# Kernel tuning notes

Measured on AMD Instinct MI355X. Metric: run time of the kernel, lower is better.

Reference implementation:

```python
import jax, jax.numpy as jnp
import numpy as np

TEMP = 1.0

def setup_inputs() -> dict:
    key = jax.random.key(0)
    k1, k2, k3, k4 = jax.random.split(key, 4)
    B, Q, K, H = 8, 1024, 4096, 512
    output = jax.random.normal(k1, (B, Q, H), dtype=jnp.float32)
    context = jax.random.normal(k2, (B, K, H), dtype=jnp.float32)
    mask = jax.random.randint(k3, (B, Q, K), 0, 2).astype(jnp.bool_)
    # linear_out: Linear(2H -> H), torch layout W: [H, 2H]
    W_out = jax.random.normal(k4, (H, 2 * H), dtype=jnp.float32) * (1.0 / np.sqrt(2 * H))
    b_out = jnp.zeros((H,), dtype=jnp.float32)
    return {"output": output, "context": context, "mask": mask, "W_out": W_out, "b_out": b_out}

def reference(output, context, mask, W_out, b_out):
    # attn scores: [B, Q, K]
    attn = jnp.einsum('bqh,bkh->bqk', output, context)
    attn = jnp.where(mask, -jnp.inf, attn)
    attn = jax.nn.softmax(attn / TEMP, axis=-1)
    # mix: [B, Q, H]
    mix = jnp.einsum('bqk,bkh->bqh', attn, context)
    combined = jnp.concatenate([mix, output], axis=-1)  # [B, Q, 2H]
    out = jnp.tanh(jnp.einsum('bqc,hc->bqh', combined, W_out) + b_out)
    return (out, attn)
```

## Files before the change

### kernel.cpp

```cpp
#include <hip/hip_runtime.h>
#include <cstdint>
#include <cstddef>

#define B_N 8
#define Q_N 1024
#define K_N 4096
#define H_N 512
#define C_N 1024
#define R_N (B_N * Q_N)

typedef short bf16x8 __attribute__((ext_vector_type(8)));
typedef float f32x4 __attribute__((ext_vector_type(4)));

typedef const void __attribute__((address_space(1))) gas_void;
typedef void __attribute__((address_space(3))) las_void;

__device__ __forceinline__ unsigned short f2bf(float f) {
    union { float f; unsigned u; } v; v.f = f;
    unsigned u = v.u;
    u += 0x7FFFu + ((u >> 16) & 1u);
    return (unsigned short)(u >> 16);
}
__device__ __forceinline__ float bf2f(unsigned short h) {
    union { unsigned u; float f; } v; v.u = ((unsigned)h) << 16;
    return v.f;
}

__device__ __forceinline__ f32x4 mfma16(bf16x8 a, bf16x8 b, f32x4 c) {
    return __builtin_amdgcn_mfma_f32_16x16x32_bf16(a, b, c, 0, 0, 0);
}

__global__ void k_split(const float* __restrict__ x, unsigned short* __restrict__ hi,
                        unsigned short* __restrict__ lo, int n4) {
    int i = blockIdx.x * 256 + threadIdx.x;
    if (i >= n4) return;
    float4 v = reinterpret_cast<const float4*>(x)[i];
    ushort4 h, l;
    h.x = f2bf(v.x); l.x = f2bf(v.x - bf2f(h.x));
    h.y = f2bf(v.y); l.y = f2bf(v.y - bf2f(h.y));
    h.z = f2bf(v.z); l.z = f2bf(v.z - bf2f(h.z));
    h.w = f2bf(v.w); l.w = f2bf(v.w - bf2f(h.w));
    reinterpret_cast<ushort4*>(hi)[i] = h;
    reinterpret_cast<ushort4*>(lo)[i] = l;
}

__global__ void k_cvt(const float* __restrict__ x, unsigned short* __restrict__ hi, int n4) {
    int i = blockIdx.x * 256 + threadIdx.x;
    if (i >= n4) return;
    float4 v = reinterpret_cast<const float4*>(x)[i];
    ushort4 h;
    h.x = f2bf(v.x); h.y = f2bf(v.y); h.z = f2bf(v.z); h.w = f2bf(v.w);
    reinterpret_cast<ushort4*>(hi)[i] = h;
}

__global__ void k_transpose(const unsigned short* __restrict__ src, unsigned short* __restrict__ dst) {
    __shared__ unsigned short tile[32][33];
    const int b = blockIdx.z;
    const int k0 = blockIdx.x * 32;
    const int h0 = blockIdx.y * 32;
    const unsigned short* s = src + (size_t)b * K_N * H_N;
    unsigned short* d = dst + (size_t)b * H_N * K_N;
    const int tx = threadIdx.x & 31;
    const int ty = threadIdx.x >> 5;
#pragma unroll
    for (int r = 0; r < 32; r += 8)
        tile[ty + r][tx] = s[(size_t)(k0 + ty + r) * H_N + (h0 + tx)];
    __syncthreads();
#pragma unroll
    for (int r = 0; r < 32; r += 8)
        d[(size_t)(h0 + ty + r) * K_N + (k0 + tx)] = tile[tx][ty + r];
}

__device__ __forceinline__ void stage_tile(const unsigned short* __restrict__ g, int ld,
                                           unsigned short* __restrict__ lds) {
    const int t = threadIdx.x;
    const int wbase = t & ~63;
#pragma unroll
    for (int i = 0; i < 2; i++) {
        int idx = i * 256 + t;
        const unsigned short* ga = g + (size_t)(idx >> 2) * ld + (idx & 3) * 8;
        unsigned short* la = lds + (size_t)(i * 256 + wbase) * 8;
        __builtin_amdgcn_global_load_lds((gas_void*)ga, (las_void*)la, 16, 0, 0);
    }
}

__global__ __launch_bounds__(256, 2)
void k_scores(const unsigned short* __restrict__ outHi, const unsigned short* __restrict__ outLo,
              const unsigned short* __restrict__ ctxHi, const unsigned short* __restrict__ ctxLo,
              float* __restrict__ S) {
    __shared__ unsigned short Ah[128 * 32], Al[128 * 32], Bh[128 * 32], Bl[128 * 32];
    const int b = blockIdx.z;
    const int q0 = blockIdx.y * 128;
    const int k0 = blockIdx.x * 128;
    const unsigned short* Ahg = outHi + ((size_t)b * Q_N + q0) * H_N;
    const unsigned short* Alg = outLo + ((size_t)b * Q_N + q0) * H_N;
    const unsigned short* Bhg = ctxHi + ((size_t)b * K_N + k0) * H_N;
    const unsigned short* Blg = ctxLo + ((size_t)b * K_N + k0) * H_N;
    const int lane = threadIdx.x & 63;
    const int w = threadIdx.x >> 6;
    const int wr = (w >> 1) * 64;
    const int wc = (w & 1) * 64;
    const int fm = lane & 15;
    const int fg = (lane >> 4) * 8;

    f32x4 acc[4][4];
#pragma unroll
    for (int i = 0; i < 4; i++)
#pragma unroll
        for (int j = 0; j < 4; j++) acc[i][j] = (f32x4){0.f, 0.f, 0.f, 0.f};

    for (int kc = 0; kc < H_N; kc += 32) {
        stage_tile(Ahg + kc, H_N, Ah);
        stage_tile(Alg + kc, H_N, Al);
        stage_tile(Bhg + kc, H_N, Bh);
        stage_tile(Blg + kc, H_N, Bl);
        __syncthreads();
        bf16x8 ah[4], al[4], bh[4], bl[4];
#pragma unroll
        for (int i = 0; i < 4; i++) {
            ah[i] = *(const bf16x8*)&Ah[(wr + i * 16 + fm) * 32 + fg];
            al[i] = *(const bf16x8*)&Al[(wr + i * 16 + fm) * 32 + fg];
            bh[i] = *(const bf16x8*)&Bh[(wc + i * 16 + fm) * 32 + fg];
            bl[i] = *(const bf16x8*)&Bl[(wc + i * 16 + fm) * 32 + fg];
        }
#pragma unroll
        for (int i = 0; i < 4; i++)
#pragma unroll
            for (int j = 0; j < 4; j++) {
                acc[i][j] = mfma16(ah[i], bh[j], acc[i][j]);
                acc[i][j] = mfma16(ah[i], bl[j], acc[i][j]);
                acc[i][j] = mfma16(al[i], bh[j], acc[i][j]);
            }
        __syncthreads();
    }
    float* Sb = S + (size_t)b * Q_N * K_N;
    const int orow = (lane >> 4) * 4;
    const int ocol = lane & 15;
#pragma unroll
    for (int i = 0; i < 4; i++)
#pragma unroll
        for (int r = 0; r < 4; r++) {
            int q = q0 + wr + i * 16 + orow + r;
            float* dst = Sb + (size_t)q * K_N + (k0 + wc + ocol);
#pragma unroll
            for (int j = 0; j < 4; j++) dst[j * 16] = acc[i][j][r];
        }
}

__global__ __launch_bounds__(256)
void k_softmax(float* __restrict__ S, const int* __restrict__ mask, unsigned short* __restrict__ pbf) {
    const size_t r = blockIdx.x;
    float* row = S + r * K_N;
    const int* mrow = mask + r * K_N;
    unsigned short* prow = pbf + r * K_N;
    const int t = threadIdx.x;

    float4 v[4];
    float lmax = -1e30f;
#pragma unroll
    for (int i = 0; i < 4; i++) {
        int idx = i * 256 + t;
        float4 s = reinterpret_cast<const float4*>(row)[idx];
        int4 mk = reinterpret_cast<const int4*>(mrow)[idx];
        s.x = mk.x ? -1e30f : s.x;
        s.y = mk.y ? -1e30f : s.y;
        s.z = mk.z ? -1e30f : s.z;
        s.w = mk.w ? -1e30f : s.w;
        v[i] = s;
        lmax = fmaxf(fmaxf(fmaxf(lmax, s.x), fmaxf(s.y, s.z)), s.w);
    }
#pragma unroll
    for (int off = 32; off >= 1; off >>= 1)
        lmax = fmaxf(lmax, __shfl_xor(lmax, off, 64));
    __shared__ float redm[4];
    __shared__ float reds[4];
    const int wv = t >> 6;
    if ((t & 63) == 0) redm[wv] = lmax;
    __syncthreads();
    const float m = fmaxf(fmaxf(redm[0], redm[1]), fmaxf(redm[2], redm[3]));

    float4 e[4];
    float lsum = 0.f;
#pragma unroll
    for (int i = 0; i < 4; i++) {
        e[i].x = __expf(v[i].x - m);
        e[i].y = __expf(v[i].y - m);
        e[i].z = __expf(v[i].z - m);
        e[i].w = __expf(v[i].w - m);
        lsum += (e[i].x + e[i].y) + (e[i].z + e[i].w);
    }
#pragma unroll
    for (int off = 32; off >= 1; off >>= 1)
        lsum += __shfl_xor(lsum, off, 64);
    if ((t & 63) == 0) reds[wv] = lsum;
    __syncthreads();
    const float inv = 1.0f / (reds[0] + reds[1] + reds[2] + reds[3]);

#pragma unroll
    for (int i = 0; i < 4; i++) {
        int idx = i * 256 + t;
        float4 p;
        p.x = e[i].x * inv; p.y = e[i].y * inv; p.z = e[i].z * inv; p.w = e[i].w * inv;
        reinterpret_cast<float4*>(row)[idx] = p;
        ushort4 pb;
        pb.x = f2bf(p.x); pb.y = f2bf(p.y); pb.z = f2bf(p.z); pb.w = f2bf(p.w);
        reinterpret_cast<ushort4*>(prow)[idx] = pb;
    }
}

__global__ __launch_bounds__(256, 2)
void k_mix(const unsigned short* __restrict__ P, const unsigned short* __restrict__ ctxT,
           unsigned short* __restrict__ mixBf) {
    __shared__ unsigned short At[128 * 32], Bt[128 * 32];
    const int b = blockIdx.z;
    const int q0 = blockIdx.y * 128;
    const int h0 = blockIdx.x * 128;
    const unsigned short* Ag = P + ((size_t)b * Q_N + q0) * K_N;
    const unsigned short* Bg = ctxT + ((size_t)b * H_N + h0) * K_N;
    const int lane = threadIdx.x & 63;
    const int w = threadIdx.x >> 6;
    const int wr = (w >> 1) * 64;
    const int wc = (w & 1) * 64;
    const int fm = lane & 15;
    const int fg = (lane >> 4) * 8;

    f32x4 acc[4][4];
#pragma unroll
    for (int i = 0; i < 4; i++)
#pragma unroll
        for (int j = 0; j < 4; j++) acc[i][j] = (f32x4){0.f, 0.f, 0.f, 0.f};

    for (int kc = 0; kc < K_N; kc += 32) {
        stage_tile(Ag + kc, K_N, At);
        stage_tile(Bg + kc, K_N, Bt);
        __syncthreads();
        bf16x8 a[4], bb[4];
#pragma unroll
        for (int i = 0; i < 4; i++) {
            a[i] = *(const bf16x8*)&At[(wr + i * 16 + fm) * 32 + fg];
            bb[i] = *(const bf16x8*)&Bt[(wc + i * 16 + fm) * 32 + fg];
        }
#pragma unroll
        for (int i = 0; i < 4; i++)
#pragma unroll
            for (int j = 0; j < 4; j++) acc[i][j] = mfma16(a[i], bb[j], acc[i][j]);
        __syncthreads();
    }
    const int orow = (lane >> 4) * 4;
    const int ocol = lane & 15;
#pragma unroll
    for (int i = 0; i < 4; i++)
#pragma unroll
        for (int r = 0; r < 4; r++) {
            int q = q0 + wr + i * 16 + orow + r;
            unsigned short* dst = mixBf + ((size_t)b * Q_N + q) * H_N + (h0 + wc + ocol);
#pragma unroll
            for (int j = 0; j < 4; j++) dst[j * 16] = f2bf(acc[i][j][r]);
        }
}

__global__ __launch_bounds__(256, 2)
void k_outlin(const unsigned short* __restrict__ mixBf, const unsigned short* __restrict__ outHi,
              const unsigned short* __restrict__ Whi, const float* __restrict__ bias,
              float* __restrict__ out) {
    __shared__ unsigned short At[128 * 32], Bt[128 * 32];
    const int r0 = blockIdx.y * 128;
    const int h0 = blockIdx.x * 128;
    const int lane = threadIdx.x & 63;
    const int w = threadIdx.x >> 6;
    const int wr = (w >> 1) * 64;
    const int wc = (w & 1) * 64;
    const int fm = lane & 15;
    const int fg = (lane >> 4) * 8;

    f32x4 acc[4][4];
#pragma unroll
    for (int i = 0; i < 4; i++)
#pragma unroll
        for (int j = 0; j < 4; j++) acc[i][j] = (f32x4){0.f, 0.f, 0.f, 0.f};

    for (int kc = 0; kc < C_N; kc += 32) {
        const unsigned short* Ag = (kc < H_N)
            ? mixBf + (size_t)r0 * H_N + kc
            : outHi + (size_t)r0 * H_N + (kc - H_N);
        stage_tile(Ag, H_N, At);
        stage_tile(Whi + (size_t)h0 * C_N + kc, C_N, Bt);
        __syncthreads();
        bf16x8 a[4], bb[4];
#pragma unroll
        for (int i = 0; i < 4; i++) {
            a[i] = *(const bf16x8*)&At[(wr + i * 16 + fm) * 32 + fg];
            bb[i] = *(const bf16x8*)&Bt[(wc + i * 16 + fm) * 32 + fg];
        }
#pragma unroll
        for (int i = 0; i < 4; i++)
#pragma unroll
            for (int j = 0; j < 4; j++) acc[i][j] = mfma16(a[i], bb[j], acc[i][j]);
        __syncthreads();
    }
    const int orow = (lane >> 4) * 4;
    const int ocol = lane & 15;
#pragma unroll
    for (int i = 0; i < 4; i++)
#pragma unroll
        for (int r = 0; r < 4; r++) {
            int rr = r0 + wr + i * 16 + orow + r;
#pragma unroll
            for (int j = 0; j < 4; j++) {
                int h = h0 + wc + j * 16 + ocol;
                float v = acc[i][j][r] + bias[h];
                out[(size_t)rr * H_N + h] = tanhf(v);
            }
        }
}

extern "C" void kernel_launch(void* const* d_in, const int* in_sizes, int n_in,
                              void* d_out, int out_size, void* d_ws, size_t ws_size,
                              hipStream_t stream) {
    const float* d_output  = (const float*)d_in[0];
    const float* d_context = (const float*)d_in[1];
    const int*   d_mask    = (const int*)d_in[2];
    const float* d_W       = (const float*)d_in[3];
    const float* d_bias    = (const float*)d_in[4];

    float* out_res = (float*)d_out;
    float* attn    = out_res + (size_t)R_N * H_N;

    char* ws = (char*)d_ws;
    unsigned short* ctxHi = (unsigned short*)ws; ws += (size_t)B_N * K_N * H_N * 2;
    unsigned short* ctxLo = (unsigned short*)ws; ws += (size_t)B_N * K_N * H_N * 2;
    unsigned short* ctxT  = (unsigned short*)ws; ws += (size_t)B_N * K_N * H_N * 2;
    unsigned short* outHi = (unsigned short*)ws; ws += (size_t)R_N * H_N * 2;
    unsigned short* outLo = (unsigned short*)ws; ws += (size_t)R_N * H_N * 2;
    unsigned short* Whi   = (unsigned short*)ws; ws += (size_t)H_N * C_N * 2;
    unsigned short* pBf   = (unsigned short*)ws; ws += (size_t)R_N * K_N * 2;
    unsigned short* mixBf = (unsigned short*)ws; ws += (size_t)R_N * H_N * 2;

    k_split<<<dim3((R_N * H_N / 4) / 256), 256, 0, stream>>>(d_output, outHi, outLo, R_N * H_N / 4);
    k_split<<<dim3((B_N * K_N * H_N / 4) / 256), 256, 0, stream>>>(d_context, ctxHi, ctxLo,
                                                                   B_N * K_N * H_N / 4);
    k_cvt<<<dim3((H_N * C_N / 4) / 256), 256, 0, stream>>>(d_W, Whi, H_N * C_N / 4);
    k_transpose<<<dim3(K_N / 32, H_N / 32, B_N), 256, 0, stream>>>(ctxHi, ctxT);

    k_scores<<<dim3(K_N / 128, Q_N / 128, B_N), 256, 0, stream>>>(outHi, outLo, ctxHi, ctxLo, attn);

    k_softmax<<<dim3(R_N), 256, 0, stream>>>(attn, d_mask, pBf);

    k_mix<<<dim3(H_N / 128, Q_N / 128, B_N), 256, 0, stream>>>(pBf, ctxT, mixBf);

    k_outlin<<<dim3(H_N / 128, R_N / 128), 256, 0, stream>>>(mixBf, outHi, Whi, d_bias, out_res);
}
```

Baseline: 570.9 us.

## Fuse context split with transpose, move masking into scores, double k_mix chunk

```diff
diff --git a/kernel.cpp b/kernel.cpp
--- a/kernel.cpp
+++ b/kernel.cpp
@@ -53,22 +53,39 @@
     reinterpret_cast<ushort4*>(hi)[i] = h;
 }
 
-__global__ void k_transpose(const unsigned short* __restrict__ src, unsigned short* __restrict__ dst) {
-    __shared__ unsigned short tile[32][33];
+__global__ __launch_bounds__(256)
+void k_prep_ctx(const float* __restrict__ ctx, unsigned short* __restrict__ ctxHi,
+                unsigned short* __restrict__ ctxLo, unsigned short* __restrict__ ctxT) {
+    __shared__ unsigned short tile[64][66];
     const int b = blockIdx.z;
-    const int k0 = blockIdx.x * 32;
-    const int h0 = blockIdx.y * 32;
-    const unsigned short* s = src + (size_t)b * K_N * H_N;
-    unsigned short* d = dst + (size_t)b * H_N * K_N;
-    const int tx = threadIdx.x & 31;
-    const int ty = threadIdx.x >> 5;
-#pragma unroll
-    for (int r = 0; r < 32; r += 8)
-        tile[ty + r][tx] = s[(size_t)(k0 + ty + r) * H_N + (h0 + tx)];
+    const int k0 = blockIdx.x * 64;
+    const int h0 = blockIdx.y * 64;
+    const int tx = threadIdx.x & 15;
+    const int ty = threadIdx.x >> 4;
+#pragma unroll
+    for (int r = 0; r < 64; r += 16) {
+        const int k = ty + r;
+        const size_t go = ((size_t)b * K_N + k0 + k) * H_N + h0 + tx * 4;
+        float4 v = *reinterpret_cast<const float4*>(ctx + go);
+        ushort4 h, l;
+        h.x = f2bf(v.x); l.x = f2bf(v.x - bf2f(h.x));
+        h.y = f2bf(v.y); l.y = f2bf(v.y - bf2f(h.y));
+        h.z = f2bf(v.z); l.z = f2bf(v.z - bf2f(h.z));
+        h.w = f2bf(v.w); l.w = f2bf(v.w - bf2f(h.w));
+        *reinterpret_cast<ushort4*>(ctxHi + go) = h;
+        *reinterpret_cast<ushort4*>(ctxLo + go) = l;
+        tile[tx * 4 + 0][k] = h.x;
+        tile[tx * 4 + 1][k] = h.y;
+        tile[tx * 4 + 2][k] = h.z;
+        tile[tx * 4 + 3][k] = h.w;
+    }
     __syncthreads();
 #pragma unroll
-    for (int r = 0; r < 32; r += 8)
-        d[(size_t)(h0 + ty + r) * K_N + (k0 + tx)] = tile[tx][ty + r];
+    for (int r = 0; r < 64; r += 16) {
+        const int h = ty + r;
+        ushort4 t4 = *reinterpret_cast<const ushort4*>(&tile[h][tx * 4]);
+        *reinterpret_cast<ushort4*>(ctxT + ((size_t)b * H_N + h0 + h) * K_N + k0 + tx * 4) = t4;
+    }
 }
 
 __device__ __forceinline__ void stage_tile(const unsigned short* __restrict__ g, int ld,
@@ -87,7 +104,7 @@
 __global__ __launch_bounds__(256, 2)
 void k_scores(const unsigned short* __restrict__ outHi, const unsigned short* __restrict__ outLo,
               const unsigned short* __restrict__ ctxHi, const unsigned short* __restrict__ ctxLo,
-              float* __restrict__ S) {
+              const int* __restrict__ mask, float* __restrict__ S) {
     __shared__ unsigned short Ah[128 * 32], Al[128 * 32], Bh[128 * 32], Bl[128 * 32];
     const int b = blockIdx.z;
     const int q0 = blockIdx.y * 128;
@@ -141,17 +158,21 @@
 #pragma unroll
         for (int r = 0; r < 4; r++) {
             int q = q0 + wr + i * 16 + orow + r;
-            float* dst = Sb + (size_t)q * K_N + (k0 + wc + ocol);
-#pragma unroll
-            for (int j = 0; j < 4; j++) dst[j * 16] = acc[i][j][r];
+            const size_t rowoff = (size_t)q * K_N + (k0 + wc + ocol);
+            float* dst = Sb + rowoff;
+            const int* mrow = mask + (size_t)b * Q_N * K_N + rowoff;
+#pragma unroll
+            for (int j = 0; j < 4; j++) {
+                float v = acc[i][j][r];
+                dst[j * 16] = mrow[j * 16] ? -1e30f : v;
+            }
         }
 }
 
 __global__ __launch_bounds__(256)
-void k_softmax(float* __restrict__ S, const int* __restrict__ mask, unsigned short* __restrict__ pbf) {
+void k_softmax(float* __restrict__ S, unsigned short* __restrict__ pbf) {
     const size_t r = blockIdx.x;
     float* row = S + r * K_N;
-    const int* mrow = mask + r * K_N;
     unsigned short* prow = pbf + r * K_N;
     const int t = threadIdx.x;
 
@@ -161,11 +182,6 @@
     for (int i = 0; i < 4; i++) {
         int idx = i * 256 + t;
         float4 s = reinterpret_cast<const float4*>(row)[idx];
-        int4 mk = reinterpret_cast<const int4*>(mrow)[idx];
-        s.x = mk.x ? -1e30f : s.x;
-        s.y = mk.y ? -1e30f : s.y;
-        s.z = mk.z ? -1e30f : s.z;
-        s.w = mk.w ? -1e30f : s.w;
         v[i] = s;
         lmax = fmaxf(fmaxf(fmaxf(lmax, s.x), fmaxf(s.y, s.z)), s.w);
     }
@@ -211,7 +227,7 @@
 __global__ __launch_bounds__(256, 2)
 void k_mix(const unsigned short* __restrict__ P, const unsigned short* __restrict__ ctxT,
            unsigned short* __restrict__ mixBf) {
-    __shared__ unsigned short At[128 * 32], Bt[128 * 32];
+    __shared__ unsigned short A0[128 * 32], A1[128 * 32], B0[128 * 32], B1[128 * 32];
     const int b = blockIdx.z;
     const int q0 = blockIdx.y * 128;
     const int h0 = blockIdx.x * 128;
@@ -230,15 +246,26 @@
 #pragma unroll
         for (int j = 0; j < 4; j++) acc[i][j] = (f32x4){0.f, 0.f, 0.f, 0.f};
 
-    for (int kc = 0; kc < K_N; kc += 32) {
-        stage_tile(Ag + kc, K_N, At);
-        stage_tile(Bg + kc, K_N, Bt);
+    for (int kc = 0; kc < K_N; kc += 64) {
+        stage_tile(Ag + kc, K_N, A0);
+        stage_tile(Ag + kc + 32, K_N, A1);
+        stage_tile(Bg + kc, K_N, B0);
+        stage_tile(Bg + kc + 32, K_N, B1);
         __syncthreads();
         bf16x8 a[4], bb[4];
 #pragma unroll
         for (int i = 0; i < 4; i++) {
-            a[i] = *(const bf16x8*)&At[(wr + i * 16 + fm) * 32 + fg];
-            bb[i] = *(const bf16x8*)&Bt[(wc + i * 16 + fm) * 32 + fg];
+            a[i] = *(const bf16x8*)&A0[(wr + i * 16 + fm) * 32 + fg];
+            bb[i] = *(const bf16x8*)&B0[(wc + i * 16 + fm) * 32 + fg];
+        }
+#pragma unroll
+        for (int i = 0; i < 4; i++)
+#pragma unroll
+            for (int j = 0; j < 4; j++) acc[i][j] = mfma16(a[i], bb[j], acc[i][j]);
+#pragma unroll
+        for (int i = 0; i < 4; i++) {
+            a[i] = *(const bf16x8*)&A1[(wr + i * 16 + fm) * 32 + fg];
+            bb[i] = *(const bf16x8*)&B1[(wc + i * 16 + fm) * 32 + fg];
         }
 #pragma unroll
         for (int i = 0; i < 4; i++)
@@ -337,14 +364,13 @@
     unsigned short* mixBf = (unsigned short*)ws; ws += (size_t)R_N * H_N * 2;
 
     k_split<<<dim3((R_N * H_N / 4) / 256), 256, 0, stream>>>(d_output, outHi, outLo, R_N * H_N / 4);
-    k_split<<<dim3((B_N * K_N * H_N / 4) / 256), 256, 0, stream>>>(d_context, ctxHi, ctxLo,
-                                                                   B_N * K_N * H_N / 4);
     k_cvt<<<dim3((H_N * C_N / 4) / 256), 256, 0, stream>>>(d_W, Whi, H_N * C_N / 4);
-    k_transpose<<<dim3(K_N / 32, H_N / 32, B_N), 256, 0, stream>>>(ctxHi, ctxT);
-
-    k_scores<<<dim3(K_N / 128, Q_N / 128, B_N), 256, 0, stream>>>(outHi, outLo, ctxHi, ctxLo, attn);
-
-    k_softmax<<<dim3(R_N), 256, 0, stream>>>(attn, d_mask, pBf);
+    k_prep_ctx<<<dim3(K_N / 64, H_N / 64, B_N), 256, 0, stream>>>(d_context, ctxHi, ctxLo, ctxT);
+
+    k_scores<<<dim3(K_N / 128, Q_N / 128, B_N), 256, 0, stream>>>(outHi, outLo, ctxHi, ctxLo,
+                                                                  d_mask, attn);
+
+    k_softmax<<<dim3(R_N), 256, 0, stream>>>(attn, pBf);
 
     k_mix<<<dim3(H_N / 128, Q_N / 128, B_N), 256, 0, stream>>>(pBf, ctxT, mixBf);
 
```

New measurement: 589.5 us. 1.03x slower.
